# Kernel tuning notes

Hardware: AMD Instinct MI355X
Metric: run time of the kernel (lower is better)

## Reference

```python
import jax, jax.numpy as jnp
import numpy as np
import math

B, S, D, H = 16, 512, 1024, 16
DH = D // H  # 64
NUM_DEG = 50
NUM_SPE = 512


def setup_inputs() -> dict:
    key = jax.random.key(0)
    ks = jax.random.split(key, 16)
    w = lambda k, shape: (jax.random.normal(k, shape, jnp.float32) * 0.02)
    return {
        "hidden_states": jax.random.normal(ks[0], (B, S, D), jnp.float32),
        "attention_mask": jnp.zeros((B, 1, 1, S), jnp.float32),
        "if_2d": 1,
        "in_degree": jax.random.randint(ks[1], (B, S), 0, NUM_DEG),
        "out_degree": jax.random.randint(ks[2], (B, S), 0, NUM_DEG),
        "spe": jax.random.randint(ks[3], (B, S, S), 0, NUM_SPE),
        "dist_3d": jax.random.normal(ks[4], (B, S), jnp.float32),
        "dist_m": jax.random.normal(ks[5], (B, S, S), jnp.float32),
        # Linear params stored as [in, out]; y = x @ W + b
        "Wq": w(ks[6], (D, D)), "bq": jnp.zeros((D,), jnp.float32),
        "Wk": w(ks[7], (D, D)), "bk": jnp.zeros((D,), jnp.float32),
        "Wv": w(ks[8], (D, D)), "bv": jnp.zeros((D,), jnp.float32),
        "W_in": w(ks[9], (NUM_DEG, D)),
        "W_out": w(ks[10], (NUM_DEG, D)),
        "W_spe": w(ks[11], (NUM_SPE, H)),
    }


def reference(hidden_states, attention_mask, if_2d, in_degree, out_degree,
              spe, dist_3d, dist_m, Wq, bq, Wk, bk, Wv, bv,
              W_in, W_out, W_spe):
    # if_2d == True branch (2D graph path). padding_idx=0 -> row 0 is zero.
    pad_mask = (jnp.arange(NUM_DEG) != 0).astype(hidden_states.dtype)[:, None]
    pos = (W_in * pad_mask)[in_degree] + (W_out * pad_mask)[out_degree]  # [B,S,D]
    bias = jnp.transpose(W_spe[spe], (0, 3, 1, 2))  # [B,S,S,H] -> [B,H,S,S]

    h = hidden_states + pos
    to_heads = lambda x: x.reshape(B, S, H, DH).transpose(0, 2, 1, 3)  # [B,H,S,DH]
    q = to_heads(h @ Wq + bq)
    k = to_heads(h @ Wk + bk)
    v = to_heads(h @ Wv + bv)

    scores = jnp.einsum('bhqd,bhkd->bhqk', q, k) / math.sqrt(DH)
    scores = scores + bias + attention_mask
    probs = jax.nn.softmax(scores, axis=-1)  # dropout p=0 (eval)
    ctx = jnp.einsum('bhqk,bhkd->bhqd', probs, v)  # [B,H,S,DH]
    ctx = ctx.transpose(0, 2, 1, 3).reshape(B, S, D)
    return ctx, probs
```

## Files before the change

### kernel.cpp

```cpp
#include <hip/hip_runtime.h>

#define Bc 16
#define Sc 512
#define Dc 1024
#define Hc 16
#define DHc 64

#define AS1 __attribute__((address_space(1)))
#define AS3 __attribute__((address_space(3)))

typedef __attribute__((ext_vector_type(8))) __bf16 bf16x8;
typedef __attribute__((ext_vector_type(4))) float f32x4;
typedef __attribute__((ext_vector_type(8))) unsigned short ushort8;

static __device__ __forceinline__ unsigned short f2bf(float f) {
  unsigned int u = __builtin_bit_cast(unsigned int, f);
  unsigned int r = (u + 0x7fffu + ((u >> 16) & 1u)) >> 16;
  return (unsigned short)r;
}
static __device__ __forceinline__ float bf2f(unsigned short u) {
  unsigned int x = ((unsigned int)u) << 16;
  return __builtin_bit_cast(float, x);
}

__global__ __launch_bounds__(256) void k_pos_add(
    const float* __restrict__ hidden, const int* __restrict__ ind,
    const int* __restrict__ outd, const float* __restrict__ Win,
    const float* __restrict__ Wout, unsigned short* __restrict__ hbf) {
  int row = blockIdx.x;
  int t = threadIdx.x;
  int id = ind[row], od = outd[row];
  float fi = (id != 0) ? 1.f : 0.f;
  float fo = (od != 0) ? 1.f : 0.f;
  float4 a = ((const float4*)(hidden + (size_t)row * Dc))[t];
  float4 x = ((const float4*)(Win + (size_t)id * Dc))[t];
  float4 y = ((const float4*)(Wout + (size_t)od * Dc))[t];
  ushort4 r;
  r.x = f2bf(a.x + fi * x.x + fo * y.x);
  r.y = f2bf(a.y + fi * x.y + fo * y.y);
  r.z = f2bf(a.z + fi * x.z + fo * y.z);
  r.w = f2bf(a.w + fi * x.w + fo * y.w);
  ((ushort4*)(hbf + (size_t)row * Dc))[t] = r;
}

__global__ __launch_bounds__(256) void k_wt(
    const float* __restrict__ Wq, const float* __restrict__ Wk,
    const float* __restrict__ Wv, unsigned short* __restrict__ Wtq,
    unsigned short* __restrict__ Wtk, unsigned short* __restrict__ Wtv) {
  const float* W = blockIdx.z == 0 ? Wq : blockIdx.z == 1 ? Wk : Wv;
  unsigned short* Wt = blockIdx.z == 0 ? Wtq : blockIdx.z == 1 ? Wtk : Wtv;
  __shared__ float tile[64][65];
  int k0 = blockIdx.y * 64, n0 = blockIdx.x * 64;
  int r = threadIdx.x >> 4, c4 = (threadIdx.x & 15) * 4;
  for (int rr = r; rr < 64; rr += 16) {
    float4 v = *(const float4*)(W + (size_t)(k0 + rr) * Dc + n0 + c4);
    tile[rr][c4 + 0] = v.x;
    tile[rr][c4 + 1] = v.y;
    tile[rr][c4 + 2] = v.z;
    tile[rr][c4 + 3] = v.w;
  }
  __syncthreads();
  for (int rr = r; rr < 64; rr += 16) {
    ushort4 o;
    o.x = f2bf(tile[c4 + 0][rr]);
    o.y = f2bf(tile[c4 + 1][rr]);
    o.z = f2bf(tile[c4 + 2][rr]);
    o.w = f2bf(tile[c4 + 3][rr]);
    *(ushort4*)(Wt + (size_t)(n0 + rr) * Dc + k0 + c4) = o;
  }
}

__global__ __launch_bounds__(256) void k_wspet(
    const float* __restrict__ Wspe, float* __restrict__ WspeT) {
  int idx = blockIdx.x * 256 + threadIdx.x;
  int h = idx >> 9, i = idx & 511;
  WspeT[idx] = Wspe[i * Hc + h];
}

__global__ __launch_bounds__(256) void k_gemm_mfma(
    const unsigned short* __restrict__ hbf,
    const unsigned short* __restrict__ Wtq, const float* __restrict__ bq,
    const unsigned short* __restrict__ Wtk, const float* __restrict__ bk,
    const unsigned short* __restrict__ Wtv, const float* __restrict__ bv,
    unsigned short* __restrict__ Qo, unsigned short* __restrict__ Ko,
    unsigned short* __restrict__ Vt) {
  int zsel = blockIdx.z;
  const unsigned short* Wt;
  const float* bias;
  if (zsel == 0) { Wt = Wtq; bias = bq; }
  else if (zsel == 1) { Wt = Wtk; bias = bk; }
  else { Wt = Wtv; bias = bv; }

  __shared__ __align__(16) unsigned short As[128 * 32];
  __shared__ __align__(16) unsigned short Bs[128 * 32];

  int tid = threadIdx.x, lane = tid & 63, wave = tid >> 6;
  int m0 = blockIdx.y * 128, n0 = blockIdx.x * 128;
  int wr = wave >> 1, wc = wave & 1;

  f32x4 acc[4][4] = {};

  int srow = lane >> 2;
  int skb = (lane & 3) * 8;
  const unsigned short* gA = hbf + (size_t)(m0 + srow) * Dc + skb;
  const unsigned short* gB = Wt + (size_t)(n0 + srow) * Dc + skb;

  int fr = lane & 15, kg = (lane >> 4) * 8;

  for (int k0 = 0; k0 < Dc; k0 += 32) {
#pragma unroll
    for (int cc = 0; cc < 2; ++cc) {
      int c = wave + cc * 4;
      __builtin_amdgcn_global_load_lds(
          (const AS1 void*)(gA + (size_t)c * 16 * Dc + k0),
          (AS3 void*)(As + c * 16 * 32), 16, 0, 0);
      __builtin_amdgcn_global_load_lds(
          (const AS1 void*)(gB + (size_t)c * 16 * Dc + k0),
          (AS3 void*)(Bs + c * 16 * 32), 16, 0, 0);
    }
    __syncthreads();

    bf16x8 af[4], bfr[4];
#pragma unroll
    for (int m = 0; m < 4; ++m)
      af[m] = *(const bf16x8*)(As + (wr * 64 + m * 16 + fr) * 32 + kg);
#pragma unroll
    for (int n = 0; n < 4; ++n)
      bfr[n] = *(const bf16x8*)(Bs + (wc * 64 + n * 16 + fr) * 32 + kg);
#pragma unroll
    for (int m = 0; m < 4; ++m)
#pragma unroll
      for (int n = 0; n < 4; ++n)
        acc[m][n] = __builtin_amdgcn_mfma_f32_16x16x32_bf16(af[m], bfr[n], acc[m][n], 0, 0, 0);
    __syncthreads();
  }

  int fq = lane >> 4;
  if (zsel < 2) {
    unsigned short* C = (zsel == 0) ? Qo : Ko;
    float scale = (zsel == 0) ? 0.125f : 1.f;
#pragma unroll
    for (int m = 0; m < 4; ++m) {
#pragma unroll
      for (int n = 0; n < 4; ++n) {
        int col = n0 + wc * 64 + n * 16 + fr;
        float bb = bias[col];
#pragma unroll
        for (int r = 0; r < 4; ++r) {
          int row = m0 + wr * 64 + m * 16 + fq * 4 + r;
          C[(size_t)row * Dc + col] = f2bf((acc[m][n][r] + bb) * scale);
        }
      }
    }
  } else {
#pragma unroll
    for (int m = 0; m < 4; ++m) {
#pragma unroll
      for (int n = 0; n < 4; ++n) {
        int col = n0 + wc * 64 + n * 16 + fr;
        int hh = col >> 6, dh = col & 63;
        float bb = bias[col];
        int row = m0 + wr * 64 + m * 16 + fq * 4;
        int bb_ = row >> 9, ss = row & 511;
        ushort4 pk;
        pk.x = f2bf(acc[m][n][0] + bb);
        pk.y = f2bf(acc[m][n][1] + bb);
        pk.z = f2bf(acc[m][n][2] + bb);
        pk.w = f2bf(acc[m][n][3] + bb);
        *(ushort4*)(Vt + ((size_t)(bb_ * Hc + hh) * DHc + dh) * Sc + ss) = pk;
      }
    }
  }
}

#define SWB 520
__global__ __launch_bounds__(256, 8) void k_attn(
    const unsigned short* __restrict__ Qb, const unsigned short* __restrict__ Kb,
    const unsigned short* __restrict__ Vt, const int* __restrict__ spe,
    const float* __restrict__ WspeT, const float* __restrict__ mask,
    float* __restrict__ probs, float* __restrict__ ctx) {
  extern __shared__ char smem[];
  unsigned short* S = (unsigned short*)smem;
  float* Wb = (float*)(smem + 16640);
  float* Rinv = (float*)(smem + 16640 + 2048);

  int tid = threadIdx.x, lane = tid & 63, w = tid >> 6;
  int fr = lane & 15, fq = lane >> 4, kg8 = fq * 8;

  int flat = blockIdx.x;
  int swz = (flat & 7) * 1024 + (flat >> 3);
  int qt = swz & 31, h = (swz >> 5) & 15, b = swz >> 9;
  int q0 = qt * 16;

  for (int i = tid; i < 512; i += 256) Wb[i] = WspeT[h * 512 + i];

  const unsigned short* qbase = Qb + (size_t)(b * Sc + q0) * Dc + h * DHc;
  bf16x8 af[2];
#pragma unroll
  for (int kk = 0; kk < 2; ++kk)
    af[kk] = *(const bf16x8*)(qbase + (size_t)fr * Dc + kk * 32 + kg8);

  const unsigned short* kbase = Kb + (size_t)(b * Sc) * Dc + h * DHc;
#pragma unroll 2
  for (int it = 0; it < 8; ++it) {
    bf16x8 kf[2];
#pragma unroll
    for (int kk = 0; kk < 2; ++kk) {
      int brow = it * 64 + w * 16 + fr;
      kf[kk] = *(const bf16x8*)(kbase + (size_t)brow * Dc + kk * 32 + kg8);
    }
    f32x4 acc = {};
#pragma unroll
    for (int kk = 0; kk < 2; ++kk)
      acc = __builtin_amdgcn_mfma_f32_16x16x32_bf16(kf[kk], af[kk], acc, 0, 0, 0);
    ushort4 pk;
    pk.x = f2bf(acc[0]); pk.y = f2bf(acc[1]);
    pk.z = f2bf(acc[2]); pk.w = f2bf(acc[3]);
    *(ushort4*)(S + fr * SWB + it * 64 + w * 16 + fq * 4) = pk;
  }
  __syncthreads();

  {
    float* pbase = probs + (size_t)((b * Hc + h) * Sc + q0) * Sc;
    float4 mk0 = *(const float4*)(mask + b * Sc + lane * 8);
    float4 mk1 = *(const float4*)(mask + b * Sc + lane * 8 + 4);
#pragma unroll 2
    for (int r4 = 0; r4 < 4; ++r4) {
      int row = w * 4 + r4;
      unsigned short* sp = S + row * SWB + lane * 8;
      const int* spp = spe + (size_t)(b * Sc + q0 + row) * Sc + lane * 8;
      ushort8 sv = *(const ushort8*)sp;
      int4 i0 = *(const int4*)(spp);
      int4 i1 = *(const int4*)(spp + 4);
      float e0 = __expf(bf2f(sv[0]) + Wb[i0.x] + mk0.x);
      float e1 = __expf(bf2f(sv[1]) + Wb[i0.y] + mk0.y);
      float e2 = __expf(bf2f(sv[2]) + Wb[i0.z] + mk0.z);
      float e3 = __expf(bf2f(sv[3]) + Wb[i0.w] + mk0.w);
      float e4 = __expf(bf2f(sv[4]) + Wb[i1.x] + mk1.x);
      float e5 = __expf(bf2f(sv[5]) + Wb[i1.y] + mk1.y);
      float e6 = __expf(bf2f(sv[6]) + Wb[i1.z] + mk1.z);
      float e7 = __expf(bf2f(sv[7]) + Wb[i1.w] + mk1.w);
      float sum = e0 + e1 + e2 + e3 + e4 + e5 + e6 + e7;
#pragma unroll
      for (int o = 32; o; o >>= 1) sum += __shfl_xor(sum, o);
      float rinv = 1.f / sum;
      ushort8 ev;
      ev[0] = f2bf(e0); ev[1] = f2bf(e1); ev[2] = f2bf(e2); ev[3] = f2bf(e3);
      ev[4] = f2bf(e4); ev[5] = f2bf(e5); ev[6] = f2bf(e6); ev[7] = f2bf(e7);
      *(ushort8*)sp = ev;
      f32x4 p0, p1;
      p0[0] = e0 * rinv; p0[1] = e1 * rinv; p0[2] = e2 * rinv; p0[3] = e3 * rinv;
      p1[0] = e4 * rinv; p1[1] = e5 * rinv; p1[2] = e6 * rinv; p1[3] = e7 * rinv;
      float* pdst = pbase + (size_t)row * Sc + lane * 8;
      __builtin_nontemporal_store(p0, (f32x4*)pdst);
      __builtin_nontemporal_store(p1, (f32x4*)(pdst + 4));
      if (lane == 0) Rinv[row] = rinv;
    }
  }
  __syncthreads();

  const unsigned short* vtbase = Vt + (size_t)(b * Hc + h) * DHc * Sc;
  f32x4 pacc = {};
#pragma unroll 2
  for (int it = 0; it < 8; ++it) {
    bf16x8 vf[2];
#pragma unroll
    for (int kk = 0; kk < 2; ++kk) {
      int dhrow = w * 16 + fr;
      vf[kk] = *(const bf16x8*)(vtbase + (size_t)dhrow * Sc + it * 64 + kk * 32 + kg8);
    }
#pragma unroll
    for (int kk = 0; kk < 2; ++kk) {
      bf16x8 pfr = *(const bf16x8*)(S + fr * SWB + it * 64 + kk * 32 + kg8);
      pacc = __builtin_amdgcn_mfma_f32_16x16x32_bf16(vf[kk], pfr, pacc, 0, 0, 0);
    }
  }

  {
    float rv = Rinv[fr];
    f32x4 o;
    o[0] = pacc[0] * rv; o[1] = pacc[1] * rv;
    o[2] = pacc[2] * rv; o[3] = pacc[3] * rv;
    __builtin_nontemporal_store(
        o, (f32x4*)(ctx + (size_t)(b * Sc + q0 + fr) * Dc + h * DHc + w * 16 + fq * 4));
  }
}

extern "C" void kernel_launch(void* const* d_in, const int* in_sizes, int n_in,
                              void* d_out, int out_size, void* d_ws, size_t ws_size,
                              hipStream_t stream) {
  const float* hidden = (const float*)d_in[0];
  const float* amask = (const float*)d_in[1];
  const int* ind = (const int*)d_in[3];
  const int* outd = (const int*)d_in[4];
  const int* spe = (const int*)d_in[5];
  const float* Wq = (const float*)d_in[8];
  const float* bq = (const float*)d_in[9];
  const float* Wk = (const float*)d_in[10];
  const float* bk = (const float*)d_in[11];
  const float* Wv = (const float*)d_in[12];
  const float* bv = (const float*)d_in[13];
  const float* Win = (const float*)d_in[14];
  const float* Wout = (const float*)d_in[15];
  const float* Wspe = (const float*)d_in[16];

  char* ws = (char*)d_ws;
  const size_t BSD = (size_t)Bc * Sc * Dc;
  unsigned short* hbf = (unsigned short*)ws;
  unsigned short* Wtq = (unsigned short*)(ws + 16u * 1048576);
  unsigned short* Wtk = (unsigned short*)(ws + 18u * 1048576);
  unsigned short* Wtv = (unsigned short*)(ws + 20u * 1048576);
  float* WspeT = (float*)(ws + 22u * 1048576);
  unsigned short* Qb = (unsigned short*)(ws + 24u * 1048576);
  unsigned short* Kb = (unsigned short*)(ws + 40u * 1048576);
  unsigned short* Vt = (unsigned short*)(ws + 56u * 1048576);
  float* ctx = (float*)d_out;
  float* probs = (float*)d_out + BSD;

  (void)hipFuncSetAttribute((const void*)k_attn,
                            hipFuncAttributeMaxDynamicSharedMemorySize, 18752);

  k_pos_add<<<dim3(Bc * Sc), 256, 0, stream>>>(hidden, ind, outd, Win, Wout, hbf);
  k_wt<<<dim3(16, 16, 3), 256, 0, stream>>>(Wq, Wk, Wv, Wtq, Wtk, Wtv);
  k_wspet<<<dim3(32), 256, 0, stream>>>(Wspe, WspeT);
  k_gemm_mfma<<<dim3(8, 64, 3), 256, 0, stream>>>(hbf, Wtq, bq, Wtk, bk, Wtv, bv, Qb, Kb, Vt);
  k_attn<<<dim3(8192), 256, 18752, stream>>>(Qb, Kb, Vt, spe, WspeT, amask, probs, ctx);
}
```

Measured before the change: 251.8 us.

## Software-pipeline K/V loads and overlap probs stores with PV matmul

Double-buffers the K and V fragment loads in register so the next tile's global loads are issued before the current MFMAs, and raises wave priority around the MFMAs. The fp32 probs write moves out of the softmax loop into the PV loop, where it is rebuilt from the bf16 exponentials in LDS times a per-row reciprocal, so the large store traffic overlaps matrix work. The PV accumulation is split into two independent accumulators. The cost is higher register pressure, and probs now derive from bf16-rounded exponentials, which slightly lowers precision.

```diff
diff --git a/kernel.cpp b/kernel.cpp
--- a/kernel.cpp
+++ b/kernel.cpp
@@ -200,38 +200,42 @@
   for (int kk = 0; kk < 2; ++kk)
     af[kk] = *(const bf16x8*)(qbase + (size_t)fr * Dc + kk * 32 + kg8);
 
-  const unsigned short* kbase = Kb + (size_t)(b * Sc) * Dc + h * DHc;
-#pragma unroll 2
+  const unsigned short* kptr =
+      Kb + (size_t)(b * Sc + w * 16 + fr) * Dc + h * DHc;
+  bf16x8 kfA0 = *(const bf16x8*)(kptr + kg8);
+  bf16x8 kfA1 = *(const bf16x8*)(kptr + 32 + kg8);
+#pragma unroll
   for (int it = 0; it < 8; ++it) {
-    bf16x8 kf[2];
-#pragma unroll
-    for (int kk = 0; kk < 2; ++kk) {
-      int brow = it * 64 + w * 16 + fr;
-      kf[kk] = *(const bf16x8*)(kbase + (size_t)brow * Dc + kk * 32 + kg8);
+    bf16x8 kfB0, kfB1;
+    if (it < 7) {
+      const unsigned short* np = kptr + (size_t)(it + 1) * 64 * Dc;
+      kfB0 = *(const bf16x8*)(np + kg8);
+      kfB1 = *(const bf16x8*)(np + 32 + kg8);
     }
     f32x4 acc = {};
-#pragma unroll
-    for (int kk = 0; kk < 2; ++kk)
-      acc = __builtin_amdgcn_mfma_f32_16x16x32_bf16(kf[kk], af[kk], acc, 0, 0, 0);
+    __builtin_amdgcn_s_setprio(1);
+    acc = __builtin_amdgcn_mfma_f32_16x16x32_bf16(kfA0, af[0], acc, 0, 0, 0);
+    acc = __builtin_amdgcn_mfma_f32_16x16x32_bf16(kfA1, af[1], acc, 0, 0, 0);
+    __builtin_amdgcn_s_setprio(0);
     ushort4 pk;
     pk.x = f2bf(acc[0]); pk.y = f2bf(acc[1]);
     pk.z = f2bf(acc[2]); pk.w = f2bf(acc[3]);
     *(ushort4*)(S + fr * SWB + it * 64 + w * 16 + fq * 4) = pk;
+    kfA0 = kfB0; kfA1 = kfB1;
   }
   __syncthreads();
 
+  float ri0, ri1, ri2, ri3;
   {
-    float* pbase = probs + (size_t)((b * Hc + h) * Sc + q0) * Sc;
+    const int* spp0 = spe + (size_t)(b * Sc + q0 + w * 4) * Sc + lane * 8;
     float4 mk0 = *(const float4*)(mask + b * Sc + lane * 8);
     float4 mk1 = *(const float4*)(mask + b * Sc + lane * 8 + 4);
-#pragma unroll 2
+#pragma unroll
     for (int r4 = 0; r4 < 4; ++r4) {
       int row = w * 4 + r4;
-      unsigned short* sp = S + row * SWB + lane * 8;
-      const int* spp = spe + (size_t)(b * Sc + q0 + row) * Sc + lane * 8;
-      ushort8 sv = *(const ushort8*)sp;
-      int4 i0 = *(const int4*)(spp);
-      int4 i1 = *(const int4*)(spp + 4);
+      int4 i0 = *(const int4*)(spp0 + (size_t)r4 * Sc);
+      int4 i1 = *(const int4*)(spp0 + (size_t)r4 * Sc + 4);
+      ushort8 sv = *(const ushort8*)(S + row * SWB + lane * 8);
       float e0 = __expf(bf2f(sv[0]) + Wb[i0.x] + mk0.x);
       float e1 = __expf(bf2f(sv[1]) + Wb[i0.y] + mk0.y);
       float e2 = __expf(bf2f(sv[2]) + Wb[i0.z] + mk0.z);
@@ -244,43 +248,59 @@
 #pragma unroll
       for (int o = 32; o; o >>= 1) sum += __shfl_xor(sum, o);
       float rinv = 1.f / sum;
+      if (r4 == 0) ri0 = rinv;
+      else if (r4 == 1) ri1 = rinv;
+      else if (r4 == 2) ri2 = rinv;
+      else ri3 = rinv;
       ushort8 ev;
       ev[0] = f2bf(e0); ev[1] = f2bf(e1); ev[2] = f2bf(e2); ev[3] = f2bf(e3);
       ev[4] = f2bf(e4); ev[5] = f2bf(e5); ev[6] = f2bf(e6); ev[7] = f2bf(e7);
-      *(ushort8*)sp = ev;
-      f32x4 p0, p1;
-      p0[0] = e0 * rinv; p0[1] = e1 * rinv; p0[2] = e2 * rinv; p0[3] = e3 * rinv;
-      p1[0] = e4 * rinv; p1[1] = e5 * rinv; p1[2] = e6 * rinv; p1[3] = e7 * rinv;
-      float* pdst = pbase + (size_t)row * Sc + lane * 8;
-      __builtin_nontemporal_store(p0, (f32x4*)pdst);
-      __builtin_nontemporal_store(p1, (f32x4*)(pdst + 4));
+      *(ushort8*)(S + row * SWB + lane * 8) = ev;
       if (lane == 0) Rinv[row] = rinv;
     }
   }
   __syncthreads();
 
-  const unsigned short* vtbase = Vt + (size_t)(b * Hc + h) * DHc * Sc;
-  f32x4 pacc = {};
-#pragma unroll 2
+  const unsigned short* vptr =
+      Vt + ((size_t)(b * Hc + h) * DHc + w * 16 + fr) * Sc;
+  float* pbase = probs + (size_t)((b * Hc + h) * Sc + q0) * Sc;
+  int prow = tid >> 4, pc0 = (tid & 15) * 4;
+  float prv = (fq == 0) ? ri0 : (fq == 1) ? ri1 : (fq == 2) ? ri2 : ri3;
+  f32x4 pacc0 = {}, pacc1 = {};
+  bf16x8 vfA0 = *(const bf16x8*)(vptr + kg8);
+  bf16x8 vfA1 = *(const bf16x8*)(vptr + 32 + kg8);
+  ushort4 svA = *(const ushort4*)(S + prow * SWB + pc0);
+#pragma unroll
   for (int it = 0; it < 8; ++it) {
-    bf16x8 vf[2];
-#pragma unroll
-    for (int kk = 0; kk < 2; ++kk) {
-      int dhrow = w * 16 + fr;
-      vf[kk] = *(const bf16x8*)(vtbase + (size_t)dhrow * Sc + it * 64 + kk * 32 + kg8);
-    }
-#pragma unroll
-    for (int kk = 0; kk < 2; ++kk) {
-      bf16x8 pfr = *(const bf16x8*)(S + fr * SWB + it * 64 + kk * 32 + kg8);
-      pacc = __builtin_amdgcn_mfma_f32_16x16x32_bf16(vf[kk], pfr, pacc, 0, 0, 0);
-    }
+    bf16x8 vfB0, vfB1;
+    ushort4 svB;
+    if (it < 7) {
+      vfB0 = *(const bf16x8*)(vptr + (it + 1) * 64 + kg8);
+      vfB1 = *(const bf16x8*)(vptr + (it + 1) * 64 + 32 + kg8);
+      svB = *(const ushort4*)(S + prow * SWB + (it + 1) * 64 + pc0);
+    }
+    {
+      f32x4 e;
+      e[0] = bf2f(svA.x) * prv; e[1] = bf2f(svA.y) * prv;
+      e[2] = bf2f(svA.z) * prv; e[3] = bf2f(svA.w) * prv;
+      __builtin_nontemporal_store(e, (f32x4*)(pbase + (size_t)prow * Sc + it * 64 + pc0));
+    }
+    bf16x8 pfr0 = *(const bf16x8*)(S + fr * SWB + it * 64 + kg8);
+    bf16x8 pfr1 = *(const bf16x8*)(S + fr * SWB + it * 64 + 32 + kg8);
+    __builtin_amdgcn_s_setprio(1);
+    pacc0 = __builtin_amdgcn_mfma_f32_16x16x32_bf16(vfA0, pfr0, pacc0, 0, 0, 0);
+    pacc1 = __builtin_amdgcn_mfma_f32_16x16x32_bf16(vfA1, pfr1, pacc1, 0, 0, 0);
+    __builtin_amdgcn_s_setprio(0);
+    vfA0 = vfB0; vfA1 = vfB1; svA = svB;
   }
 
   {
     float rv = Rinv[fr];
     f32x4 o;
-    o[0] = pacc[0] * rv; o[1] = pacc[1] * rv;
-    o[2] = pacc[2] * rv; o[3] = pacc[3] * rv;
+    o[0] = (pacc0[0] + pacc1[0]) * rv;
+    o[1] = (pacc0[1] + pacc1[1]) * rv;
+    o[2] = (pacc0[2] + pacc1[2]) * rv;
+    o[3] = (pacc0[3] + pacc1[3]) * rv;
     __builtin_nontemporal_store(
         o, (f32x4*)(ctx + (size_t)(b * Sc + q0 + fr) * Dc + h * DHc + w * 16 + fq * 4));
   }
```

New measurement: 241.9 us. 3.9% less time.
